# Kernel optimization log

Hardware: AMD Instinct MI355X
Metric: run time of the kernel (lower is better)

## Reference

```python
import jax, jax.numpy as jnp
import numpy as np

EMBED = 1024
HEADS = 16
B, T = 4, 2048


def setup_inputs() -> dict:
    key = jax.random.key(0)
    k1, k2, k3, k4, k5 = jax.random.split(key, 5)
    s_in = 1.0 / np.sqrt(EMBED)
    return {
        "x": jax.random.normal(k1, (B, T, EMBED), dtype=jnp.float32),
        "w_qkv": jax.random.uniform(k2, (3 * EMBED, EMBED), jnp.float32, -s_in, s_in),
        "b_qkv": jax.random.uniform(k3, (3 * EMBED,), jnp.float32, -s_in, s_in),
        "w_proj": jax.random.uniform(k4, (EMBED, EMBED), jnp.float32, -s_in, s_in),
        "b_proj": jax.random.uniform(k5, (EMBED,), jnp.float32, -s_in, s_in),
    }


def reference(x, w_qkv, b_qkv, w_proj, b_proj):
    Bz, Tz, C = x.shape
    nh = HEADS
    hs = C // nh
    qkv = jnp.einsum('btc,oc->bto', x, w_qkv) + b_qkv  # [B,T,3C]
    q, k, v = jnp.split(qkv, 3, axis=-1)
    # [B, nh, T, hs]
    q = q.reshape(Bz, Tz, nh, hs).transpose(0, 2, 1, 3)
    k = k.reshape(Bz, Tz, nh, hs).transpose(0, 2, 1, 3)
    v = v.reshape(Bz, Tz, nh, hs).transpose(0, 2, 1, 3)
    scale = 1.0 / np.sqrt(hs).astype(np.float32)
    att = jnp.einsum('bhqd,bhkd->bhqk', q, k) * scale
    causal_mask = jnp.tril(jnp.ones((Tz, Tz), dtype=bool))
    att = jnp.where(causal_mask[None, None], att, jnp.finfo(att.dtype).min)
    att = jax.nn.softmax(att, axis=-1)
    y = jnp.einsum('bhqk,bhkd->bhqd', att, v)
    y = y.transpose(0, 2, 1, 3).reshape(Bz, Tz, C)
    return jnp.einsum('btc,oc->bto', y, w_proj) + b_proj
```

## Files before the change

kernel.cpp:

```cpp
#include <hip/hip_runtime.h>

typedef __bf16 bf16x8 __attribute__((ext_vector_type(8)));
typedef float f32x4 __attribute__((ext_vector_type(4)));

#define DI __device__ __forceinline__

#define WAIT_VMCNT(N)                                        \
  do {                                                       \
    __builtin_amdgcn_sched_barrier(0);                       \
    asm volatile("s_waitcnt vmcnt(" #N ")" ::: "memory");    \
    __builtin_amdgcn_sched_barrier(0);                       \
  } while (0)

DI unsigned short f2bf(float f) {
  unsigned int u = __float_as_uint(f);
  u += 0x7FFFu + ((u >> 16) & 1u);
  return (unsigned short)(u >> 16);
}

DI unsigned cvt_pk_bf16(float a, float b) {
  unsigned r;
  asm("v_cvt_pk_bf16_f32 %0, %1, %2" : "=v"(r) : "v"(a), "v"(b));
  return r;
}

DI float exp2_fast(float x) {
  float r;
  asm("v_exp_f32 %0, %1" : "=v"(r) : "v"(x));
  return r;
}

DI void fence() { asm volatile("" ::: "memory"); }
DI void bar() { fence(); __builtin_amdgcn_s_barrier(); fence(); }

DI bf16x8 ld16(const void* p) {
  union { uint4 u; bf16x8 b; } c;
  c.u = *reinterpret_cast<const uint4*>(p);
  return c.b;
}

DI f32x4 mfma16(bf16x8 a, bf16x8 b, f32x4 c) {
  return __builtin_amdgcn_mfma_f32_16x16x32_bf16(a, b, c, 0, 0, 0);
}

DI void gload_lds16(const void* g, void* l) {
  __builtin_amdgcn_global_load_lds(
      (const __attribute__((address_space(1))) unsigned int*)g,
      (__attribute__((address_space(3))) unsigned int*)l, 16, 0, 0);
}

__global__ void cvt_all(const float* __restrict__ x, const float* __restrict__ wq,
                        const float* __restrict__ wp,
                        unsigned short* __restrict__ xb, unsigned short* __restrict__ wqb,
                        unsigned short* __restrict__ wpb) {
  int i = blockIdx.x * blockDim.x + threadIdx.x;
  const float* s;
  unsigned short* d;
  int off;
  if (i < 2097152) { s = x; d = xb; off = i; }
  else if (i < 2097152 + 786432) { s = wq; d = wqb; off = i - 2097152; }
  else { s = wp; d = wpb; off = i - (2097152 + 786432); }
  float4 v = reinterpret_cast<const float4*>(s)[off];
  uint2 o;
  o.x = cvt_pk_bf16(v.x, v.y);
  o.y = cvt_pk_bf16(v.z, v.w);
  reinterpret_cast<uint2*>(d)[off] = o;
}

template <int N, int MODE>
__global__ __launch_bounds__(256)
void gemm_bt(const unsigned short* __restrict__ A,
             const unsigned short* __restrict__ W,
             const float* __restrict__ bias,
             float* __restrict__ out,
             unsigned short* __restrict__ qo,
             unsigned short* __restrict__ ko,
             unsigned short* __restrict__ vo) {
  constexpr int K = 1024;
  __shared__ __align__(16) char smem[32768];
  char* Asm = smem;
  char* Bsm = smem + 16384;
  const int tid = threadIdx.x;
  const int ln = tid & 63;
  const int w  = tid >> 6;
  const int wm = w >> 1, wn = w & 1;
  const int g = ln >> 4, q = ln & 15;
  const int m0 = blockIdx.x * 128;
  const int n0 = blockIdx.y * 128;

  f32x4 acc[4][4] = {};

  for (int kt = 0; kt < K / 64; ++kt) {
    if (kt) bar();
#pragma unroll
    for (int i = 0; i < 4; ++i) {
      const int chunk = i * 4 + w;
      const int o = chunk * 1024 + ln * 16;
      const int row = o >> 7;
      const int colb = (o & 127) ^ ((row & 7) << 4);
      gload_lds16((const char*)A + ((size_t)(m0 + row) * K + kt * 64) * 2 + colb,
                  Asm + chunk * 1024);
      gload_lds16((const char*)W + ((size_t)(n0 + row) * K + kt * 64) * 2 + colb,
                  Bsm + chunk * 1024);
    }
    WAIT_VMCNT(0);
    bar();
#pragma unroll
    for (int ks = 0; ks < 2; ++ks) {
      bf16x8 av[4], bv[4];
#pragma unroll
      for (int mf = 0; mf < 4; ++mf) {
        const int row = wm * 64 + mf * 16 + q;
        av[mf] = ld16(Asm + ((row * 128 + ks * 64 + g * 16) ^ ((row & 7) << 4)));
      }
#pragma unroll
      for (int nf = 0; nf < 4; ++nf) {
        const int row = wn * 64 + nf * 16 + q;
        bv[nf] = ld16(Bsm + ((row * 128 + ks * 64 + g * 16) ^ ((row & 7) << 4)));
      }
#pragma unroll
      for (int mf = 0; mf < 4; ++mf)
#pragma unroll
        for (int nf = 0; nf < 4; ++nf)
          acc[mf][nf] = mfma16(av[mf], bv[nf], acc[mf][nf]);
    }
  }

#pragma unroll
  for (int nf = 0; nf < 4; ++nf) {
    const int col = n0 + wn * 64 + nf * 16 + q;
    const float bv = bias[col];
#pragma unroll
    for (int mf = 0; mf < 4; ++mf) {
      const int rbase = m0 + wm * 64 + mf * 16 + g * 4;
      if constexpr (MODE == 0) {
#pragma unroll
        for (int r = 0; r < 4; ++r)
          out[(size_t)(rbase + r) * N + col] = acc[mf][nf][r] + bv;
      } else {
        const int b = rbase >> 11, t0 = rbase & 2047;
        if (col < 1024) {
          const int h = col >> 6, d = col & 63;
          unsigned short* qp = qo + ((((size_t)b * 16 + h) << 11) + t0) * 64 + d;
#pragma unroll
          for (int r = 0; r < 4; ++r)
            qp[r * 64] = f2bf((acc[mf][nf][r] + bv) * 0.18033688011112042f);
        } else if (col < 2048) {
          const int c = col - 1024;
          const int h = c >> 6, d = c & 63;
          unsigned short* kp = ko + ((((size_t)b * 16 + h) << 11) + t0) * 64 + d;
#pragma unroll
          for (int r = 0; r < 4; ++r)
            kp[r * 64] = f2bf(acc[mf][nf][r] + bv);
        } else {
          const int c = col - 2048;
          const int h = c >> 6, d = c & 63;
          uint2 pk;
          pk.x = cvt_pk_bf16(acc[mf][nf][0] + bv, acc[mf][nf][1] + bv);
          pk.y = cvt_pk_bf16(acc[mf][nf][2] + bv, acc[mf][nf][3] + bv);
          *(uint2*)(vo + ((((size_t)b * 16 + h) << 6) + d) * 2048 + t0) = pk;
        }
      }
    }
  }
}

DI int asb(int row) { return ((row & 3) | (((row >> 3) & 1) << 2)) << 4; }

__global__ __launch_bounds__(256, 4)
void attn_fwd(const unsigned short* __restrict__ Qb,
              const unsigned short* __restrict__ Kb,
              const unsigned short* __restrict__ Vtb,
              unsigned short* __restrict__ Yb) {
  __shared__ __align__(16) char smem[32768];
  const int tid = threadIdx.x;
  const int ln = tid & 63;
  const int w = tid >> 6;
  const int g = ln >> 4, q = ln & 15;
  const int bh = blockIdx.x;
  const int pair = blockIdx.y;
  const size_t base = (size_t)bh * 2048 * 64;
  const int b = bh >> 4, h = bh & 15;
  const int qrow = (q & 3) + 8 * (q >> 2);

  auto stage = [&](int j, int buf) {
    char* Kd = smem + buf * 16384;
    char* Vd = Kd + 8192;
    const int kv0 = j << 6;
    const char* Kg = (const char*)(Kb + base + (size_t)kv0 * 64);
    const char* Vg = (const char*)(Vtb + base) + kv0 * 2;
#pragma unroll
    for (int i = 0; i < 2; ++i) {
      const int chunk = i * 4 + w;
      const int o = chunk * 1024 + ln * 16;
      const int row = o >> 7;
      const int colb = (o & 127) ^ asb(row);
      gload_lds16(Kg + row * 128 + colb, Kd + chunk * 1024);
      gload_lds16(Vg + (size_t)row * 4096 + colb, Vd + chunk * 1024);
    }
  };

  auto tile_step = [&](const bf16x8* qf, float& m_run, float& l_run, f32x4* yt,
                       int qw, int kv0, const char* Ksm, const char* Vsm) {
    f32x4 st[4] = {};
    __builtin_amdgcn_s_setprio(1);
#pragma unroll
    for (int f = 0; f < 4; ++f) {
      const int row = qrow + 4 * (f & 1) + 32 * (f >> 1);
      const int swz = asb(row);
      const bf16x8 a0 = ld16(Ksm + ((row * 128 + g * 16) ^ swz));
      const bf16x8 a1 = ld16(Ksm + ((row * 128 + 64 + g * 16) ^ swz));
      st[f] = mfma16(a0, qf[0], st[f]);
      st[f] = mfma16(a1, qf[1], st[f]);
    }
    __builtin_amdgcn_s_setprio(0);
    if (kv0 + 63 > qw) {
#pragma unroll
      for (int f = 0; f < 4; ++f) {
        const int kvb = kv0 + 8 * g + 4 * (f & 1) + 32 * (f >> 1);
#pragma unroll
        for (int r = 0; r < 4; ++r)
          if (kvb + r > qw + q) st[f][r] = -INFINITY;
      }
    }
    {
      float vmax = -INFINITY;
#pragma unroll
      for (int f = 0; f < 4; ++f) {
        const f32x4 v = st[f];
        vmax = fmaxf(fmaxf(vmax, fmaxf(v[0], v[1])), fmaxf(v[2], v[3]));
      }
      vmax = fmaxf(vmax, __shfl_xor(vmax, 16));
      vmax = fmaxf(vmax, __shfl_xor(vmax, 32));
      const float mo = m_run;
      if (__any(vmax > mo)) {
        const float mn = fmaxf(mo, vmax);
        const float corr = exp2_fast(mo - mn);
        m_run = mn;
        l_run *= corr;
#pragma unroll
        for (int mfd = 0; mfd < 4; ++mfd) yt[mfd] *= corr;
      }
      const float mcur = m_run;
      float ls = 0.f;
#pragma unroll
      for (int f = 0; f < 4; ++f) {
#pragma unroll
        for (int r = 0; r < 4; ++r) {
          st[f][r] = exp2_fast(st[f][r] - mcur);
          ls += st[f][r];
        }
      }
      ls += __shfl_xor(ls, 16);
      ls += __shfl_xor(ls, 32);
      l_run += ls;
    }
    union { uint4 u; bf16x8 bb; } pb0, pb1;
    pb0.u.x = cvt_pk_bf16(st[0][0], st[0][1]);
    pb0.u.y = cvt_pk_bf16(st[0][2], st[0][3]);
    pb0.u.z = cvt_pk_bf16(st[1][0], st[1][1]);
    pb0.u.w = cvt_pk_bf16(st[1][2], st[1][3]);
    pb1.u.x = cvt_pk_bf16(st[2][0], st[2][1]);
    pb1.u.y = cvt_pk_bf16(st[2][2], st[2][3]);
    pb1.u.z = cvt_pk_bf16(st[3][0], st[3][1]);
    pb1.u.w = cvt_pk_bf16(st[3][2], st[3][3]);
    __builtin_amdgcn_s_setprio(1);
#pragma unroll
    for (int mfd = 0; mfd < 4; ++mfd) {
      const int vrow = mfd * 16 + q;
      const int swz = asb(vrow);
      const bf16x8 v0 = ld16(Vsm + ((vrow * 128 + g * 16) ^ swz));
      const bf16x8 v1 = ld16(Vsm + ((vrow * 128 + 64 + g * 16) ^ swz));
      yt[mfd] = mfma16(v0, pb0.bb, yt[mfd]);
      yt[mfd] = mfma16(v1, pb1.bb, yt[mfd]);
    }
    __builtin_amdgcn_s_setprio(0);
  };

  auto epilogue = [&](float l_run, const f32x4* yt, int qw) {
    const float inv = 1.f / l_run;
    const int qr = qw + q;
    unsigned short* yp = Yb + (size_t)(b * 2048 + qr) * 1024 + h * 64;
#pragma unroll
    for (int mfd = 0; mfd < 4; ++mfd) {
      uint2 o2;
      o2.x = cvt_pk_bf16(yt[mfd][0] * inv, yt[mfd][1] * inv);
      o2.y = cvt_pk_bf16(yt[mfd][2] * inv, yt[mfd][3] * inv);
      *(uint2*)(yp + mfd * 16 + g * 4) = o2;
    }
  };

  const int hi = 31 - pair, lo = pair;
  const int qw_hi = hi * 64 + w * 16;
  const int qw_lo = lo * 64 + w * 16;

  bf16x8 qh[2], ql[2];
#pragma unroll
  for (int kf = 0; kf < 2; ++kf) {
    qh[kf] = ld16(Qb + base + (size_t)(qw_hi + q) * 64 + kf * 32 + g * 8);
    ql[kf] = ld16(Qb + base + (size_t)(qw_lo + q) * 64 + kf * 32 + g * 8);
  }
  WAIT_VMCNT(0);

  float m_hi = -INFINITY, l_hi = 0.f, m_lo = -INFINITY, l_lo = 0.f;
  f32x4 yh[4] = {}, yl[4] = {};

  const int njv = hi + 1;
  stage(0, 0);
  for (int j = 0; j < njv; ++j) {
    if (j + 1 < njv) {
      stage(j + 1, (j + 1) & 1);
      WAIT_VMCNT(4);
    } else {
      WAIT_VMCNT(0);
    }
    bar();

    const int kv0 = j << 6;
    const char* Ksm = smem + (j & 1) * 16384;
    const char* Vsm = Ksm + 8192;
    tile_step(qh, m_hi, l_hi, yh, qw_hi, kv0, Ksm, Vsm);
    if (j <= lo)
      tile_step(ql, m_lo, l_lo, yl, qw_lo, kv0, Ksm, Vsm);
    bar();
  }

  epilogue(l_hi, yh, qw_hi);
  epilogue(l_lo, yl, qw_lo);
}

extern "C" void kernel_launch(void* const* d_in, const int* in_sizes, int n_in,
                              void* d_out, int out_size, void* d_ws, size_t ws_size,
                              hipStream_t stream) {
  const float* x      = (const float*)d_in[0];
  const float* w_qkv  = (const float*)d_in[1];
  const float* b_qkv  = (const float*)d_in[2];
  const float* w_proj = (const float*)d_in[3];
  const float* b_proj = (const float*)d_in[4];
  float* out = (float*)d_out;
  char* ws = (char*)d_ws;

  unsigned short* xb  = (unsigned short*)(ws);
  unsigned short* wqb = (unsigned short*)(ws + (size_t)(16 << 20));
  unsigned short* wpb = (unsigned short*)(ws + (size_t)(22 << 20));
  unsigned short* Qb  = (unsigned short*)(ws + (size_t)(24 << 20));
  unsigned short* Kb  = (unsigned short*)(ws + (size_t)(40 << 20));
  unsigned short* Vtb = (unsigned short*)(ws + (size_t)(56 << 20));
  unsigned short* Yb  = (unsigned short*)(ws + (size_t)(72 << 20));

  cvt_all<<<12288, 256, 0, stream>>>(x, w_qkv, w_proj, xb, wqb, wpb);
  gemm_bt<3072, 1><<<dim3(64, 24), 256, 0, stream>>>(xb, wqb, b_qkv, nullptr, Qb, Kb, Vtb);
  attn_fwd<<<dim3(64, 16), 256, 0, stream>>>(Qb, Kb, Vtb, Yb);
  gemm_bt<1024, 0><<<dim3(64, 8), 256, 0, stream>>>(Yb, wpb, b_proj, out, nullptr, nullptr, nullptr);
}
```

Measured before the change: 160.8 us.

## Replace QKV GEMM with 256x256-tile, 8-wave, double-buffered pipelined kernel

Adds a dedicated QKV projection kernel that uses 256x256 output tiles, 512 threads and 128 KB of dynamic LDS. It double-buffers direct global-to-LDS loads, splitting each K-step into quarter stages interleaved with MFMA phases, and raises wave priority around the MFMAs. The goal is more data reuse per loaded tile and overlap of memory latency with compute in the largest GEMM. The cost is one block per CU from the LDS footprint, a grid of only 384 blocks, and LDS reads without the earlier XOR swizzle, which may cause bank conflicts.

```diff
diff --git a/kernel.cpp b/kernel.cpp
--- a/kernel.cpp
+++ b/kernel.cpp
@@ -67,15 +67,125 @@
   reinterpret_cast<uint2*>(d)[off] = o;
 }
 
-template <int N, int MODE>
+__global__ __launch_bounds__(512, 2)
+void gemm_qkv8(const unsigned short* __restrict__ A,
+               const unsigned short* __restrict__ W,
+               const float* __restrict__ bias,
+               unsigned short* __restrict__ qo,
+               unsigned short* __restrict__ ko,
+               unsigned short* __restrict__ vo) {
+  extern __shared__ char smem[];
+  constexpr int K = 1024;
+  const int tid = threadIdx.x;
+  const int ln = tid & 63, w = tid >> 6;
+  const int wm = w >> 2, wn = w & 3;
+  const int g = ln >> 4, q = ln & 15;
+  const int m0 = blockIdx.x * 256;
+  const int n0 = blockIdx.y * 256;
+
+  f32x4 acc[8][4] = {};
+
+  auto stage = [&](int t, int part) {
+    const int isB = part & 1, kh = part >> 1;
+    char* dst = smem + (t & 1) * 65536 + isB * 32768 + kh * 16384 + w * 2048;
+    const unsigned short* src = isB ? W : A;
+    const int mn0 = isB ? n0 : m0;
+#pragma unroll
+    for (int j = 0; j < 2; ++j) {
+      const int o = w * 2048 + j * 1024 + ln * 16;
+      gload_lds16((const char*)src +
+                      ((size_t)(mn0 + (o >> 6)) * K + t * 64 + kh * 32) * 2 + (o & 63),
+                  dst + j * 1024);
+    }
+  };
+
+  bf16x8 bfr[4];
+  auto phase = [&](const char* slot, int kh, int mh) {
+    const char* Ab = slot + kh * 16384;
+    const char* Bb = slot + 32768 + kh * 16384;
+    if (mh == 0) {
+#pragma unroll
+      for (int nf = 0; nf < 4; ++nf)
+        bfr[nf] = ld16(Bb + (wn * 64 + nf * 16 + q) * 64 + g * 16);
+    }
+    bf16x8 af[4];
+#pragma unroll
+    for (int a = 0; a < 4; ++a)
+      af[a] = ld16(Ab + (wm * 128 + (mh * 4 + a) * 16 + q) * 64 + g * 16);
+    asm volatile("s_waitcnt lgkmcnt(0)" ::: "memory");
+    __builtin_amdgcn_sched_barrier(0);
+    __builtin_amdgcn_s_setprio(1);
+#pragma unroll
+    for (int a = 0; a < 4; ++a)
+#pragma unroll
+      for (int nf = 0; nf < 4; ++nf)
+        acc[mh * 4 + a][nf] = mfma16(af[a], bfr[nf], acc[mh * 4 + a][nf]);
+    __builtin_amdgcn_s_setprio(0);
+  };
+
+  stage(0, 0); stage(0, 1); stage(0, 2); stage(0, 3);
+  char* s0 = smem;
+  char* s1 = smem + 65536;
+
+  for (int i = 0; i < 7; ++i) {
+    const int ta = 2 * i + 1, tb = 2 * i + 2;
+    stage(ta, 0); WAIT_VMCNT(6); bar(); phase(s0, 0, 0);
+    stage(ta, 1);               bar(); phase(s0, 0, 1);
+    stage(ta, 2); WAIT_VMCNT(6); bar(); phase(s0, 1, 0);
+    stage(ta, 3);               bar(); phase(s0, 1, 1);
+    stage(tb, 0); WAIT_VMCNT(6); bar(); phase(s1, 0, 0);
+    stage(tb, 1);               bar(); phase(s1, 0, 1);
+    stage(tb, 2); WAIT_VMCNT(6); bar(); phase(s1, 1, 0);
+    stage(tb, 3);               bar(); phase(s1, 1, 1);
+  }
+  stage(15, 0); WAIT_VMCNT(6); bar(); phase(s0, 0, 0);
+  stage(15, 1);               bar(); phase(s0, 0, 1);
+  stage(15, 2); WAIT_VMCNT(6); bar(); phase(s0, 1, 0);
+  stage(15, 3);               bar(); phase(s0, 1, 1);
+  WAIT_VMCNT(4); bar(); phase(s1, 0, 0);
+  bar();                phase(s1, 0, 1);
+  WAIT_VMCNT(0); bar(); phase(s1, 1, 0);
+  bar();                phase(s1, 1, 1);
+
+#pragma unroll
+  for (int nf = 0; nf < 4; ++nf) {
+    const int col = n0 + wn * 64 + nf * 16 + q;
+    const float bv = bias[col];
+#pragma unroll
+    for (int mf = 0; mf < 8; ++mf) {
+      const int rbase = m0 + wm * 128 + mf * 16 + g * 4;
+      const int b = rbase >> 11, t0 = rbase & 2047;
+      if (col < 1024) {
+        const int h = col >> 6, d = col & 63;
+        unsigned short* qp = qo + ((((size_t)b * 16 + h) << 11) + t0) * 64 + d;
+#pragma unroll
+        for (int r = 0; r < 4; ++r)
+          qp[r * 64] = f2bf((acc[mf][nf][r] + bv) * 0.18033688011112042f);
+      } else if (col < 2048) {
+        const int c = col - 1024;
+        const int h = c >> 6, d = c & 63;
+        unsigned short* kp = ko + ((((size_t)b * 16 + h) << 11) + t0) * 64 + d;
+#pragma unroll
+        for (int r = 0; r < 4; ++r)
+          kp[r * 64] = f2bf(acc[mf][nf][r] + bv);
+      } else {
+        const int c = col - 2048;
+        const int h = c >> 6, d = c & 63;
+        uint2 pk;
+        pk.x = cvt_pk_bf16(acc[mf][nf][0] + bv, acc[mf][nf][1] + bv);
+        pk.y = cvt_pk_bf16(acc[mf][nf][2] + bv, acc[mf][nf][3] + bv);
+        *(uint2*)(vo + ((((size_t)b * 16 + h) << 6) + d) * 2048 + t0) = pk;
+      }
+    }
+  }
+}
+
+template <int N>
 __global__ __launch_bounds__(256)
 void gemm_bt(const unsigned short* __restrict__ A,
              const unsigned short* __restrict__ W,
              const float* __restrict__ bias,
-             float* __restrict__ out,
-             unsigned short* __restrict__ qo,
-             unsigned short* __restrict__ ko,
-             unsigned short* __restrict__ vo) {
+             float* __restrict__ out) {
   constexpr int K = 1024;
   __shared__ __align__(16) char smem[32768];
   char* Asm = smem;
@@ -133,34 +243,9 @@
 #pragma unroll
     for (int mf = 0; mf < 4; ++mf) {
       const int rbase = m0 + wm * 64 + mf * 16 + g * 4;
-      if constexpr (MODE == 0) {
-#pragma unroll
-        for (int r = 0; r < 4; ++r)
-          out[(size_t)(rbase + r) * N + col] = acc[mf][nf][r] + bv;
-      } else {
-        const int b = rbase >> 11, t0 = rbase & 2047;
-        if (col < 1024) {
-          const int h = col >> 6, d = col & 63;
-          unsigned short* qp = qo + ((((size_t)b * 16 + h) << 11) + t0) * 64 + d;
-#pragma unroll
-          for (int r = 0; r < 4; ++r)
-            qp[r * 64] = f2bf((acc[mf][nf][r] + bv) * 0.18033688011112042f);
-        } else if (col < 2048) {
-          const int c = col - 1024;
-          const int h = c >> 6, d = c & 63;
-          unsigned short* kp = ko + ((((size_t)b * 16 + h) << 11) + t0) * 64 + d;
-#pragma unroll
-          for (int r = 0; r < 4; ++r)
-            kp[r * 64] = f2bf(acc[mf][nf][r] + bv);
-        } else {
-          const int c = col - 2048;
-          const int h = c >> 6, d = c & 63;
-          uint2 pk;
-          pk.x = cvt_pk_bf16(acc[mf][nf][0] + bv, acc[mf][nf][1] + bv);
-          pk.y = cvt_pk_bf16(acc[mf][nf][2] + bv, acc[mf][nf][3] + bv);
-          *(uint2*)(vo + ((((size_t)b * 16 + h) << 6) + d) * 2048 + t0) = pk;
-        }
-      }
+#pragma unroll
+      for (int r = 0; r < 4; ++r)
+        out[(size_t)(rbase + r) * N + col] = acc[mf][nf][r] + bv;
     }
   }
 }
@@ -348,8 +433,11 @@
   unsigned short* Vtb = (unsigned short*)(ws + (size_t)(56 << 20));
   unsigned short* Yb  = (unsigned short*)(ws + (size_t)(72 << 20));
 
+  hipFuncSetAttribute((const void*)gemm_qkv8,
+                      hipFuncAttributeMaxDynamicSharedMemorySize, 131072);
+
   cvt_all<<<12288, 256, 0, stream>>>(x, w_qkv, w_proj, xb, wqb, wpb);
-  gemm_bt<3072, 1><<<dim3(64, 24), 256, 0, stream>>>(xb, wqb, b_qkv, nullptr, Qb, Kb, Vtb);
+  gemm_qkv8<<<dim3(32, 12), 512, 131072, stream>>>(xb, wqb, b_qkv, Qb, Kb, Vtb);
   attn_fwd<<<dim3(64, 16), 256, 0, stream>>>(Qb, Kb, Vtb, Yb);
-  gemm_bt<1024, 0><<<dim3(64, 8), 256, 0, stream>>>(Yb, wpb, b_proj, out, nullptr, nullptr, nullptr);
-}
+  gemm_bt<1024><<<dim3(64, 8), 256, 0, stream>>>(Yb, wpb, b_proj, out);
+}
```

Result: slower. 185.2 us (+15.2%).
